# Performance work log

Hardware: AMD Instinct MI355X
Metric: run time of the kernel (lower is better)

Reference implementation:

```python
import jax, jax.numpy as jnp
import numpy as np

B, N, C = 1, 256, 128        # batch, n_res, norm_channel
H, AC = 4, 32                # num_head, attention_channel


def setup_inputs() -> dict:
    key = jax.random.key(0)
    ks = jax.random.split(key, 9)
    s = 0.02
    return {
        "act": jax.random.normal(ks[0], (B, N, N, C), jnp.float32),
        "mask": jnp.ones((B, N, N), jnp.float32),
        "ln_g": jnp.ones((C,), jnp.float32),
        "ln_b": jnp.zeros((C,), jnp.float32),
        "wq": (jax.random.normal(ks[1], (C, H * AC), jnp.float32) * s),
        "wk": (jax.random.normal(ks[2], (C, H * AC), jnp.float32) * s),
        "wv": (jax.random.normal(ks[3], (C, H * AC), jnp.float32) * s),
        "w2d": (jax.random.normal(ks[4], (C, H), jnp.float32) * s),
        "wg": (jax.random.normal(ks[5], (C, H * AC), jnp.float32) * s),
        "bg": jnp.zeros((H * AC,), jnp.float32),
        "wo": (jax.random.normal(ks[6], (H * AC, C), jnp.float32) * s),
        "bo": jnp.zeros((C,), jnp.float32),
    }


def reference(act, mask, ln_g, ln_b, wq, wk, wv, w2d, wg, bg, wo, bo):
    eps = 1e-5
    mu = jnp.mean(act, axis=-1, keepdims=True)
    var = jnp.mean(jnp.square(act - mu), axis=-1, keepdims=True)
    a = (act - mu) * jax.lax.rsqrt(var + eps) * ln_g + ln_b  # LayerNorm

    b_, m_, i_, _ = a.shape
    q = (a @ wq).reshape(b_, m_, i_, H, AC)
    k = (a @ wk).reshape(b_, m_, i_, H, AC)
    v = (a @ wv).reshape(b_, m_, i_, H, AC)

    factor = 1.0 / np.sqrt(AC).astype(np.float32)
    # mask bias: [b, m, 1, 1, j]
    bias = (1e9 * (mask - 1.0))[:, :, None, None, :]
    aff = jnp.einsum('bmihc,bmjhc->bmhij', q * factor, k) + bias

    # pair bias: [b, h, i, j], broadcast over m (torch trailing-dim broadcast, b=1)
    nb = jnp.einsum('bijc,ch->bhij', a, w2d)
    weights = jax.nn.softmax(aff + nb[:, None], axis=-1)  # [b,m,h,i,j]

    g = jax.nn.sigmoid(a @ wg + bg).reshape(b_, m_, i_, H, AC)
    out = jnp.einsum('bmhqk,bmkhc->bmqhc', weights, v) * g  # [b,m,q,h,c]
    return out.reshape(b_, m_, i_, H * AC) @ wo + bo
```

## Files before the change

### kernel.cpp

```cpp
#include <hip/hip_runtime.h>
#include <hip/hip_fp16.h>
#include <math.h>


#define NRES 256
#define CCH  128
#define NROWS (NRES * NRES)
#define FACTOR 0.17677669529663687f
#define LOG2E  1.44269504088896341f

typedef __attribute__((ext_vector_type(8))) __bf16 bf16x8;
typedef __attribute__((ext_vector_type(4))) float f32x4;

__device__ __forceinline__ f32x4 mfma16(bf16x8 a, bf16x8 b, f32x4 c) {
    return __builtin_amdgcn_mfma_f32_16x16x32_bf16(a, b, c, 0, 0, 0);
}

union PK4 { __bf16 b[4]; uint2 u2; };

__device__ __forceinline__ void hilo(float x, __bf16& h, __bf16& l) {
    h = (__bf16)x;
    l = (__bf16)(x - (float)h);
}

__global__ __launch_bounds__(256) void nbprep_kernel(
    const float* __restrict__ act, const float* __restrict__ ln_g,
    const float* __restrict__ ln_b, const float* __restrict__ w2d,
    const float* __restrict__ wq, const float* __restrict__ wk,
    const float* __restrict__ wv, const float* __restrict__ wg,
    const float* __restrict__ wo,
    __bf16* __restrict__ wph, __bf16* __restrict__ wpl,
    float* __restrict__ nbP)
{
    const int t = threadIdx.x;
    if (blockIdx.x >= 512) {
        const int gid = (blockIdx.x - 512) * 256 + t;
        const int wid = gid >> 11;
        const int rem = gid & 2047;
        const int nstrip = rem >> 8;
        const int kf = (rem >> 6) & 3;
        const int lane = rem & 63;
        const int l15 = lane & 15, quad = lane >> 4;
        const float* W = (wid == 0) ? wq : (wid == 1) ? wk :
                         (wid == 2) ? wv : (wid == 3) ? wg : wo;
        const float scale = (wid == 0) ? FACTOR * LOG2E : 1.0f;
        bf16x8 hb, lb;
        #pragma unroll
        for (int e = 0; e < 8; ++e) {
            int k = kf * 32 + quad * 8 + e;
            int n = nstrip * 16 + l15;
            float v = W[k * CCH + n] * scale;
            __bf16 h, l; hilo(v, h, l);
            hb[e] = h; lb[e] = l;
        }
        *(bf16x8*)&wph[(size_t)gid * 8] = hb;
        *(bf16x8*)&wpl[(size_t)gid * 8] = lb;
        return;
    }
    const int w = t >> 6, lane = t & 63;
    const int r0w = blockIdx.x * 128 + w * 32;
    const int row = lane >> 1, half = lane & 1;
    const int grow = r0w + row;
    const float* __restrict__ xp = act + (size_t)grow * CCH + half * 64;
    float4 x4[16];
    #pragma unroll
    for (int c = 0; c < 16; ++c) x4[c] = *(const float4*)(xp + c * 4);
    float s = 0.f, sq = 0.f;
    #pragma unroll
    for (int c = 0; c < 16; ++c) {
        s  += (x4[c].x + x4[c].y) + (x4[c].z + x4[c].w);
        sq += x4[c].x * x4[c].x + x4[c].y * x4[c].y +
              x4[c].z * x4[c].z + x4[c].w * x4[c].w;
    }
    s  += __shfl_xor(s, 1, 64);
    sq += __shfl_xor(sq, 1, 64);
    float mu  = s * (1.0f / CCH);
    float var = fmaf(sq, 1.0f / CCH, -mu * mu);
    float rs  = rsqrtf(var + 1e-5f);
    float nb[4] = {0.f, 0.f, 0.f, 0.f};
    const float4* __restrict__ w2d4 = (const float4*)w2d;
    #pragma unroll
    for (int c = 0; c < 16; ++c) {
        float4 g4 = *(const float4*)&ln_g[half * 64 + c * 4];
        float4 b4 = *(const float4*)&ln_b[half * 64 + c * 4];
        float* xv = (float*)&x4[c];
        float* gv = (float*)&g4;
        float* bv = (float*)&b4;
        #pragma unroll
        for (int e = 0; e < 4; ++e) {
            float av = fmaf((xv[e] - mu) * rs, gv[e], bv[e]);
            float4 wv = w2d4[half * 64 + c * 4 + e];
            nb[0] = fmaf(av, wv.x, nb[0]);
            nb[1] = fmaf(av, wv.y, nb[1]);
            nb[2] = fmaf(av, wv.z, nb[2]);
            nb[3] = fmaf(av, wv.w, nb[3]);
        }
    }
    #pragma unroll
    for (int hh = 0; hh < 4; ++hh)
        nb[hh] += __shfl_xor(nb[hh], 1, 64);
    if (half == 0) {
        const int i = grow >> 8, j = grow & 255;
        #pragma unroll
        for (int hh = 0; hh < 4; ++hh) {
            size_t f = ((size_t)hh << 14) + ((size_t)(i >> 4) << 10) +
                       ((size_t)(j >> 4) << 6) + ((size_t)((j >> 2) & 3) << 4) +
                       (i & 15);
            nbP[f * 4 + (j & 3)] = nb[hh] * LOG2E;
        }
    }
}

__device__ __forceinline__ void proj16(const bf16x8* A0,
    const __bf16* __restrict__ Bh, int lane, f32x4* acc)
{
    #pragma unroll
    for (int n = 0; n < 8; ++n) acc[n] = (f32x4){0.f, 0.f, 0.f, 0.f};
    #pragma unroll
    for (int kf = 0; kf < 4; ++kf)
        #pragma unroll
        for (int n = 0; n < 8; ++n) {
            bf16x8 bh = *(const bf16x8*)&Bh[(size_t)((n * 4 + kf) * 64 + lane) * 8];
            acc[n] = mfma16(A0[kf], bh, acc[n]);
        }
}

__global__ __launch_bounds__(1024) void mega_kernel(
    const float* __restrict__ act, const float* __restrict__ ln_g,
    const float* __restrict__ ln_b, const __bf16* __restrict__ wph,
    const __bf16* __restrict__ wpl, const float* __restrict__ bg,
    const float* __restrict__ mask, const float* __restrict__ nbP,
    const float* __restrict__ bo, float* __restrict__ out)
{
    __shared__ __align__(16) char smem[158720];
    const int t = threadIdx.x, w = t >> 6, lane = t & 63;
    const int l15 = lane & 15, quad = lane >> 4;
    const int m = blockIdx.x;
    __bf16* const Kl = (__bf16*)smem;
    __bf16* const aH = (__bf16*)(smem + w * 4352);
    __bf16* const VT = (__bf16*)(smem + 69632);
    __bf16* const ph = (__bf16*)(smem + 137216 + w * 1280);
    float*  const biasrow = (float*)(smem + 157696);

    if (t < 256)
        biasrow[t] = fmaf(1.442695e9f, mask[m * NRES + t] - 1.0f, -4.0f * LOG2E);

    {
        const int row = lane >> 2, g = lane & 3;
        const int grow = m * NRES + w * 16 + row;
        const float* __restrict__ xp = act + (size_t)grow * CCH + g * 32;
        float4 x4[8];
        #pragma unroll
        for (int c = 0; c < 8; ++c) x4[c] = *(const float4*)(xp + c * 4);
        float s = 0.f, sq = 0.f;
        #pragma unroll
        for (int c = 0; c < 8; ++c) {
            s  += (x4[c].x + x4[c].y) + (x4[c].z + x4[c].w);
            sq += x4[c].x * x4[c].x + x4[c].y * x4[c].y +
                  x4[c].z * x4[c].z + x4[c].w * x4[c].w;
        }
        #pragma unroll
        for (int o = 1; o <= 2; o <<= 1) {
            s  += __shfl_xor(s, o, 64);
            sq += __shfl_xor(sq, o, 64);
        }
        float mu  = s * (1.0f / CCH);
        float var = fmaf(sq, 1.0f / CCH, -mu * mu);
        float rs  = rsqrtf(var + 1e-5f);
        #pragma unroll
        for (int c2 = 0; c2 < 4; ++c2) {
            bf16x8 pk;
            #pragma unroll
            for (int cc = 0; cc < 2; ++cc) {
                const int c = c2 * 2 + cc;
                float4 g4 = *(const float4*)&ln_g[g * 32 + c * 4];
                float4 b4 = *(const float4*)&ln_b[g * 32 + c * 4];
                float* xv = (float*)&x4[c];
                float* gv = (float*)&g4;
                float* bv = (float*)&b4;
                #pragma unroll
                for (int e = 0; e < 4; ++e)
                    pk[cc * 4 + e] = (__bf16)fmaf((xv[e] - mu) * rs, gv[e], bv[e]);
            }
            *(bf16x8*)&aH[row * 136 + g * 32 + c2 * 8] = pk;
        }
    }

    bf16x8 A0[4];
    #pragma unroll
    for (int kf = 0; kf < 4; ++kf)
        A0[kf] = *(const bf16x8*)&aH[l15 * 136 + kf * 32 + quad * 8];

    f32x4 acc[8];
    bf16x8 Qh[4];
    uint2  greg[4][2];

    proj16(A0, wph, lane, acc);
    {
        __bf16* const sth = aH;
        #pragma unroll
        for (int n = 0; n < 8; ++n)
            #pragma unroll
            for (int r = 0; r < 4; ++r)
                sth[(quad * 4 + r) * 136 + n * 16 + l15] = (__bf16)acc[n][r];
        #pragma unroll
        for (int h = 0; h < 4; ++h)
            Qh[h] = *(const bf16x8*)&sth[l15 * 136 + h * 32 + quad * 8];
    }

    proj16(A0, wph + 3 * 16384, lane, acc);
    {
        __half* const sthH = (__half*)aH;
        #pragma unroll
        for (int n = 0; n < 8; ++n)
            #pragma unroll
            for (int r = 0; r < 4; ++r) {
                float v = acc[n][r] + bg[n * 16 + l15];
                sthH[(quad * 4 + r) * 136 + n * 16 + l15] =
                    (__half)(1.0f / (1.0f + __expf(-v)));
            }
        #pragma unroll
        for (int h = 0; h < 4; ++h)
            #pragma unroll
            for (int c = 0; c < 2; ++c)
                greg[h][c] =
                    *(const uint2*)&sthH[l15 * 136 + h * 32 + c * 16 + quad * 4];
    }

    proj16(A0, wph + 1 * 16384, lane, acc);
    #pragma unroll
    for (int n = 0; n < 8; ++n)
        #pragma unroll
        for (int r = 0; r < 4; ++r)
            aH[(quad * 4 + r) * 136 + n * 16 + l15] = (__bf16)acc[n][r];

    proj16(A0, wph + 2 * 16384, lane, acc);
    #pragma unroll
    for (int n = 0; n < 8; ++n)
        #pragma unroll
        for (int r = 0; r < 4; ++r)
            VT[(n * 16 + l15) * 264 + w * 16 + quad * 4 + r] = (__bf16)acc[n][r];

    __syncthreads();

    uint2 ovh[4][2], ovl[4][2];
    #pragma unroll
    for (int h = 0; h < 4; ++h) {
        f32x4 O[2];
        O[0] = (f32x4){0.f, 0.f, 0.f, 0.f};
        O[1] = (f32x4){0.f, 0.f, 0.f, 0.f};
        float ls = 0.f;
        float4 nb_a[2], nb_b[2];
        #pragma unroll
        for (int js = 0; js < 2; ++js)
            nb_a[js] = *(const float4*)&nbP[
                ((size_t)h * 16384 + (size_t)w * 1024 +
                 (size_t)js * 64 + quad * 16 + l15) * 4];
        #pragma unroll 1
        for (int jb = 0; jb < NRES; jb += 32) {
            bf16x8 Kh[2];
            #pragma unroll
            for (int js = 0; js < 2; ++js)
                Kh[js] = *(const bf16x8*)&Kl[(jb + js * 16 + l15) * 136 +
                                             h * 32 + quad * 8];
            bf16x8 Vh2[2];
            #pragma unroll
            for (int c = 0; c < 2; ++c)
                Vh2[c] = *(const bf16x8*)&VT[(h * 32 + c * 16 + l15) * 264 +
                                             jb + quad * 8];
            const int jn = (jb + 32 < NRES) ? (jb >> 4) + 2 : 0;
            #pragma unroll
            for (int js = 0; js < 2; ++js)
                nb_b[js] = *(const float4*)&nbP[
                    ((size_t)h * 16384 + (size_t)w * 1024 +
                     (size_t)(jn + js) * 64 + quad * 16 + l15) * 4];
            #pragma unroll
            for (int js = 0; js < 2; ++js) {
                f32x4 S = (f32x4){0.f, 0.f, 0.f, 0.f};
                S = mfma16(Kh[js], Qh[h], S);
                float4 nb4 = nb_a[js];
                float4 mb4 = *(const float4*)&biasrow[jb + js * 16 + quad * 4];
                float p0 = exp2f(S[0] + nb4.x + mb4.x);
                float p1 = exp2f(S[1] + nb4.y + mb4.y);
                float p2 = exp2f(S[2] + nb4.z + mb4.z);
                float p3 = exp2f(S[3] + nb4.w + mb4.w);
                ls += (p0 + p1) + (p2 + p3);
                PK4 hh;
                hh.b[0] = (__bf16)p0; hh.b[1] = (__bf16)p1;
                hh.b[2] = (__bf16)p2; hh.b[3] = (__bf16)p3;
                *(uint2*)&ph[l15 * 40 + js * 16 + quad * 4] = hh.u2;
            }
            bf16x8 Ph = *(const bf16x8*)&ph[l15 * 40 + quad * 8];
            #pragma unroll
            for (int c = 0; c < 2; ++c)
                O[c] = mfma16(Vh2[c], Ph, O[c]);
            nb_a[0] = nb_b[0];
            nb_a[1] = nb_b[1];
        }
        ls += __shfl_xor(ls, 16, 64);
        ls += __shfl_xor(ls, 32, 64);
        float inv = 1.0f / ls;
        #pragma unroll
        for (int c = 0; c < 2; ++c) {
            const __half* gh = (const __half*)&greg[h][c];
            PK4 hh, lo;
            #pragma unroll
            for (int r = 0; r < 4; ++r) {
                float v = O[c][r] * inv * (float)gh[r];
                __bf16 hb; __bf16 lb; hilo(v, hb, lb);
                hh.b[r] = hb; lo.b[r] = lb;
            }
            ovh[h][c] = hh.u2;
            ovl[h][c] = lo.u2;
        }
    }
    __syncthreads();

    {
        __bf16* const sth = aH;
        #pragma unroll
        for (int h = 0; h < 4; ++h)
            #pragma unroll
            for (int c = 0; c < 2; ++c)
                *(uint2*)&sth[l15 * 136 + h * 32 + c * 16 + quad * 4] = ovh[h][c];
        bf16x8 Ah0[4];
        #pragma unroll
        for (int kf = 0; kf < 4; ++kf)
            Ah0[kf] = *(const bf16x8*)&sth[l15 * 136 + kf * 32 + quad * 8];
        #pragma unroll
        for (int h = 0; h < 4; ++h)
            #pragma unroll
            for (int c = 0; c < 2; ++c)
                *(uint2*)&sth[l15 * 136 + h * 32 + c * 16 + quad * 4] = ovl[h][c];
        bf16x8 Al0[4];
        #pragma unroll
        for (int kf = 0; kf < 4; ++kf)
            Al0[kf] = *(const bf16x8*)&sth[l15 * 136 + kf * 32 + quad * 8];

        const __bf16* __restrict__ Bh = wph + (size_t)4 * 16384;
        const __bf16* __restrict__ Bl = wpl + (size_t)4 * 16384;
        #pragma unroll
        for (int n = 0; n < 8; ++n) acc[n] = (f32x4){0.f, 0.f, 0.f, 0.f};
        #pragma unroll
        for (int kf = 0; kf < 4; ++kf)
            #pragma unroll
            for (int n = 0; n < 8; ++n) {
                size_t boff = (size_t)((n * 4 + kf) * 64 + lane) * 8;
                bf16x8 bh = *(const bf16x8*)&Bh[boff];
                bf16x8 bl = *(const bf16x8*)&Bl[boff];
                acc[n] = mfma16(Ah0[kf], bh, acc[n]);
                acc[n] = mfma16(Ah0[kf], bl, acc[n]);
                acc[n] = mfma16(Al0[kf], bh, acc[n]);
            }

        const size_t rbase = (size_t)m * NRES + w * 16;
        #pragma unroll
        for (int n = 0; n < 8; ++n) {
            float b = bo[n * 16 + l15];
            #pragma unroll
            for (int r = 0; r < 4; ++r)
                out[(rbase + quad * 4 + r) * CCH + n * 16 + l15] = acc[n][r] + b;
        }
    }
}

extern "C" void kernel_launch(void* const* d_in, const int* in_sizes, int n_in,
                              void* d_out, int out_size, void* d_ws, size_t ws_size,
                              hipStream_t stream)
{
    const float* act  = (const float*)d_in[0];
    const float* mask = (const float*)d_in[1];
    const float* ln_g = (const float*)d_in[2];
    const float* ln_b = (const float*)d_in[3];
    const float* wq   = (const float*)d_in[4];
    const float* wk   = (const float*)d_in[5];
    const float* wv   = (const float*)d_in[6];
    const float* w2d  = (const float*)d_in[7];
    const float* wg   = (const float*)d_in[8];
    const float* bg   = (const float*)d_in[9];
    const float* wo   = (const float*)d_in[10];
    const float* bo   = (const float*)d_in[11];
    float* out = (float*)d_out;

    float* nbP = (float*)d_ws;
    __bf16* wph = (__bf16*)(nbP + 4 * NROWS);
    __bf16* wpl = wph + 5 * 16384;

    nbprep_kernel<<<552, 256, 0, stream>>>(
        act, ln_g, ln_b, w2d, wq, wk, wv, wg, wo, wph, wpl, nbP);
    mega_kernel<<<256, 1024, 0, stream>>>(
        act, ln_g, ln_b, wph, wpl, bg, mask, nbP, bo, out);
}
```

Baseline: 193.6 us.

## Move LayerNorm into pre-kernel and feed bf16 normalized activations to mega kernel

The pre-kernel now computes LayerNorm once per row with 8 threads per row, writes the normalized activations as bf16 to a workspace buffer, and reuses them for the pair-bias projection. The mega kernel loads its A fragments straight from this bf16 buffer, so it no longer re-reads fp32 act, recomputes LayerNorm, or round-trips through shared memory. The V transpose store is packed into 64-bit writes and nbP indexing is simplified. The cost is an extra 16 MB bf16 write plus read, and a larger pre-kernel grid.

```diff
diff --git a/kernel.cpp b/kernel.cpp
--- a/kernel.cpp
+++ b/kernel.cpp
@@ -23,18 +23,18 @@
     l = (__bf16)(x - (float)h);
 }
 
-__global__ __launch_bounds__(256) void nbprep_kernel(
+__global__ __launch_bounds__(256) void pre_kernel(
     const float* __restrict__ act, const float* __restrict__ ln_g,
     const float* __restrict__ ln_b, const float* __restrict__ w2d,
     const float* __restrict__ wq, const float* __restrict__ wk,
     const float* __restrict__ wv, const float* __restrict__ wg,
     const float* __restrict__ wo,
     __bf16* __restrict__ wph, __bf16* __restrict__ wpl,
-    float* __restrict__ nbP)
+    float* __restrict__ nbP, __bf16* __restrict__ aLN)
 {
     const int t = threadIdx.x;
-    if (blockIdx.x >= 512) {
-        const int gid = (blockIdx.x - 512) * 256 + t;
+    if (blockIdx.x >= 2048) {
+        const int gid = (blockIdx.x - 2048) * 256 + t;
         const int wid = gid >> 11;
         const int rem = gid & 2047;
         const int nstrip = rem >> 8;
@@ -57,49 +57,64 @@
         *(bf16x8*)&wpl[(size_t)gid * 8] = lb;
         return;
     }
-    const int w = t >> 6, lane = t & 63;
-    const int r0w = blockIdx.x * 128 + w * 32;
-    const int row = lane >> 1, half = lane & 1;
-    const int grow = r0w + row;
-    const float* __restrict__ xp = act + (size_t)grow * CCH + half * 64;
-    float4 x4[16];
-    #pragma unroll
-    for (int c = 0; c < 16; ++c) x4[c] = *(const float4*)(xp + c * 4);
+    const int ridx = t >> 3, g = t & 7;
+    const int grow = blockIdx.x * 32 + ridx;
+    const float* __restrict__ xp = act + (size_t)grow * CCH + g * 16;
+    float4 x4[4];
+    #pragma unroll
+    for (int c = 0; c < 4; ++c) x4[c] = *(const float4*)(xp + c * 4);
     float s = 0.f, sq = 0.f;
     #pragma unroll
-    for (int c = 0; c < 16; ++c) {
+    for (int c = 0; c < 4; ++c) {
         s  += (x4[c].x + x4[c].y) + (x4[c].z + x4[c].w);
         sq += x4[c].x * x4[c].x + x4[c].y * x4[c].y +
               x4[c].z * x4[c].z + x4[c].w * x4[c].w;
     }
-    s  += __shfl_xor(s, 1, 64);
-    sq += __shfl_xor(sq, 1, 64);
+    #pragma unroll
+    for (int o = 1; o <= 4; o <<= 1) {
+        s  += __shfl_xor(s, o, 64);
+        sq += __shfl_xor(sq, o, 64);
+    }
     float mu  = s * (1.0f / CCH);
     float var = fmaf(sq, 1.0f / CCH, -mu * mu);
     float rs  = rsqrtf(var + 1e-5f);
-    float nb[4] = {0.f, 0.f, 0.f, 0.f};
-    const float4* __restrict__ w2d4 = (const float4*)w2d;
-    #pragma unroll
-    for (int c = 0; c < 16; ++c) {
-        float4 g4 = *(const float4*)&ln_g[half * 64 + c * 4];
-        float4 b4 = *(const float4*)&ln_b[half * 64 + c * 4];
+    float av[16];
+    #pragma unroll
+    for (int c = 0; c < 4; ++c) {
+        float4 g4 = *(const float4*)&ln_g[g * 16 + c * 4];
+        float4 b4 = *(const float4*)&ln_b[g * 16 + c * 4];
         float* xv = (float*)&x4[c];
         float* gv = (float*)&g4;
         float* bv = (float*)&b4;
         #pragma unroll
-        for (int e = 0; e < 4; ++e) {
-            float av = fmaf((xv[e] - mu) * rs, gv[e], bv[e]);
-            float4 wv = w2d4[half * 64 + c * 4 + e];
-            nb[0] = fmaf(av, wv.x, nb[0]);
-            nb[1] = fmaf(av, wv.y, nb[1]);
-            nb[2] = fmaf(av, wv.z, nb[2]);
-            nb[3] = fmaf(av, wv.w, nb[3]);
-        }
-    }
-    #pragma unroll
-    for (int hh = 0; hh < 4; ++hh)
-        nb[hh] += __shfl_xor(nb[hh], 1, 64);
-    if (half == 0) {
+        for (int e = 0; e < 4; ++e)
+            av[c * 4 + e] = fmaf((xv[e] - mu) * rs, gv[e], bv[e]);
+    }
+    bf16x8 o1, o2;
+    #pragma unroll
+    for (int e = 0; e < 8; ++e) {
+        o1[e] = (__bf16)av[e];
+        o2[e] = (__bf16)av[8 + e];
+    }
+    *(bf16x8*)&aLN[(size_t)grow * CCH + g * 16] = o1;
+    *(bf16x8*)&aLN[(size_t)grow * CCH + g * 16 + 8] = o2;
+
+    float nb[4] = {0.f, 0.f, 0.f, 0.f};
+    const float4* __restrict__ w2d4 = (const float4*)w2d;
+    #pragma unroll
+    for (int c = 0; c < 16; ++c) {
+        float4 wv = w2d4[g * 16 + c];
+        nb[0] = fmaf(av[c], wv.x, nb[0]);
+        nb[1] = fmaf(av[c], wv.y, nb[1]);
+        nb[2] = fmaf(av[c], wv.z, nb[2]);
+        nb[3] = fmaf(av[c], wv.w, nb[3]);
+    }
+    #pragma unroll
+    for (int o = 1; o <= 4; o <<= 1)
+        #pragma unroll
+        for (int hh = 0; hh < 4; ++hh)
+            nb[hh] += __shfl_xor(nb[hh], o, 64);
+    if (g == 0) {
         const int i = grow >> 8, j = grow & 255;
         #pragma unroll
         for (int hh = 0; hh < 4; ++hh) {
@@ -126,8 +141,7 @@
 }
 
 __global__ __launch_bounds__(1024) void mega_kernel(
-    const float* __restrict__ act, const float* __restrict__ ln_g,
-    const float* __restrict__ ln_b, const __bf16* __restrict__ wph,
+    const __bf16* __restrict__ aLN, const __bf16* __restrict__ wph,
     const __bf16* __restrict__ wpl, const float* __restrict__ bg,
     const float* __restrict__ mask, const float* __restrict__ nbP,
     const float* __restrict__ bo, float* __restrict__ out)
@@ -145,51 +159,14 @@
     if (t < 256)
         biasrow[t] = fmaf(1.442695e9f, mask[m * NRES + t] - 1.0f, -4.0f * LOG2E);
 
-    {
-        const int row = lane >> 2, g = lane & 3;
-        const int grow = m * NRES + w * 16 + row;
-        const float* __restrict__ xp = act + (size_t)grow * CCH + g * 32;
-        float4 x4[8];
-        #pragma unroll
-        for (int c = 0; c < 8; ++c) x4[c] = *(const float4*)(xp + c * 4);
-        float s = 0.f, sq = 0.f;
-        #pragma unroll
-        for (int c = 0; c < 8; ++c) {
-            s  += (x4[c].x + x4[c].y) + (x4[c].z + x4[c].w);
-            sq += x4[c].x * x4[c].x + x4[c].y * x4[c].y +
-                  x4[c].z * x4[c].z + x4[c].w * x4[c].w;
-        }
-        #pragma unroll
-        for (int o = 1; o <= 2; o <<= 1) {
-            s  += __shfl_xor(s, o, 64);
-            sq += __shfl_xor(sq, o, 64);
-        }
-        float mu  = s * (1.0f / CCH);
-        float var = fmaf(sq, 1.0f / CCH, -mu * mu);
-        float rs  = rsqrtf(var + 1e-5f);
-        #pragma unroll
-        for (int c2 = 0; c2 < 4; ++c2) {
-            bf16x8 pk;
-            #pragma unroll
-            for (int cc = 0; cc < 2; ++cc) {
-                const int c = c2 * 2 + cc;
-                float4 g4 = *(const float4*)&ln_g[g * 32 + c * 4];
-                float4 b4 = *(const float4*)&ln_b[g * 32 + c * 4];
-                float* xv = (float*)&x4[c];
-                float* gv = (float*)&g4;
-                float* bv = (float*)&b4;
-                #pragma unroll
-                for (int e = 0; e < 4; ++e)
-                    pk[cc * 4 + e] = (__bf16)fmaf((xv[e] - mu) * rs, gv[e], bv[e]);
-            }
-            *(bf16x8*)&aH[row * 136 + g * 32 + c2 * 8] = pk;
-        }
-    }
-
     bf16x8 A0[4];
-    #pragma unroll
-    for (int kf = 0; kf < 4; ++kf)
-        A0[kf] = *(const bf16x8*)&aH[l15 * 136 + kf * 32 + quad * 8];
+    {
+        const __bf16* __restrict__ ap =
+            aLN + ((size_t)m * NRES + w * 16 + l15) * CCH;
+        #pragma unroll
+        for (int kf = 0; kf < 4; ++kf)
+            A0[kf] = *(const bf16x8*)&ap[kf * 32 + quad * 8];
+    }
 
     f32x4 acc[8];
     bf16x8 Qh[4];
@@ -235,11 +212,16 @@
             aH[(quad * 4 + r) * 136 + n * 16 + l15] = (__bf16)acc[n][r];
 
     proj16(A0, wph + 2 * 16384, lane, acc);
-    #pragma unroll
-    for (int n = 0; n < 8; ++n)
-        #pragma unroll
-        for (int r = 0; r < 4; ++r)
-            VT[(n * 16 + l15) * 264 + w * 16 + quad * 4 + r] = (__bf16)acc[n][r];
+    {
+        const int jcol = w * 16 + quad * 4;
+        #pragma unroll
+        for (int n = 0; n < 8; ++n) {
+            PK4 pv;
+            #pragma unroll
+            for (int r = 0; r < 4; ++r) pv.b[r] = (__bf16)acc[n][r];
+            *(uint2*)&VT[(n * 16 + l15) * 264 + jcol] = pv.u2;
+        }
+    }
 
     __syncthreads();
 
@@ -250,12 +232,11 @@
         O[0] = (f32x4){0.f, 0.f, 0.f, 0.f};
         O[1] = (f32x4){0.f, 0.f, 0.f, 0.f};
         float ls = 0.f;
+        const int nbbase = (h * 16384 + w * 1024 + quad * 16 + l15) * 4;
         float4 nb_a[2], nb_b[2];
         #pragma unroll
         for (int js = 0; js < 2; ++js)
-            nb_a[js] = *(const float4*)&nbP[
-                ((size_t)h * 16384 + (size_t)w * 1024 +
-                 (size_t)js * 64 + quad * 16 + l15) * 4];
+            nb_a[js] = *(const float4*)(nbP + nbbase + (js << 8));
         #pragma unroll 1
         for (int jb = 0; jb < NRES; jb += 32) {
             bf16x8 Kh[2];
@@ -271,9 +252,7 @@
             const int jn = (jb + 32 < NRES) ? (jb >> 4) + 2 : 0;
             #pragma unroll
             for (int js = 0; js < 2; ++js)
-                nb_b[js] = *(const float4*)&nbP[
-                    ((size_t)h * 16384 + (size_t)w * 1024 +
-                     (size_t)(jn + js) * 64 + quad * 16 + l15) * 4];
+                nb_b[js] = *(const float4*)(nbP + nbbase + ((jn + js) << 8));
             #pragma unroll
             for (int js = 0; js < 2; ++js) {
                 f32x4 S = (f32x4){0.f, 0.f, 0.f, 0.f};
@@ -385,9 +364,10 @@
     float* nbP = (float*)d_ws;
     __bf16* wph = (__bf16*)(nbP + 4 * NROWS);
     __bf16* wpl = wph + 5 * 16384;
-
-    nbprep_kernel<<<552, 256, 0, stream>>>(
-        act, ln_g, ln_b, w2d, wq, wk, wv, wg, wo, wph, wpl, nbP);
+    __bf16* aLN = wpl + 5 * 16384;
+
+    pre_kernel<<<2088, 256, 0, stream>>>(
+        act, ln_g, ln_b, w2d, wq, wk, wv, wg, wo, wph, wpl, nbP, aLN);
     mega_kernel<<<256, 1024, 0, stream>>>(
-        act, ln_g, ln_b, wph, wpl, bg, mask, nbP, bo, out);
-}
+        aLN, wph, wpl, bg, mask, nbP, bo, out);
+}
```

Result: faster. 189.0 us (-2.3%).
